# Kernel tuning notes

Hardware: AMD Instinct MI355X
Metric: run time of the kernel (lower is better)

The kernel has to match this reference:

```python
import jax, jax.numpy as jnp
import numpy as np

DEGREE = 10

def _chebyshev_basis(x, degree):
    # x: [B, F] -> basis: [B, F, degree+1] via T0=1, T1=t, Tk=2t*T_{k-1}-T_{k-2}
    t = jnp.tanh(x)
    polys = [jnp.ones_like(t), t]
    for _ in range(2, degree + 1):
        polys.append(2.0 * t * polys[-1] - polys[-2])
    return jnp.stack(polys, axis=-1)

def setup_inputs() -> dict:
    key = jax.random.key(0)
    k1, k2, k3, k4 = jax.random.split(key, 4)
    B, F_IN, F_OUT, D = 8192, 1024, 1024, DEGREE
    x = jax.random.normal(k1, (B, F_IN), dtype=jnp.float32)
    coeff_mean = jax.random.normal(k2, (F_IN, F_OUT, D + 1), dtype=jnp.float32) * 0.05
    coeff_log_var = jnp.full((F_IN, F_OUT, D + 1), -5.0, dtype=jnp.float32)
    base_weight = jax.random.normal(k3, (F_IN, F_OUT), dtype=jnp.float32) * 0.05
    # reparameterization noise, n_samples=1
    eps = jax.random.normal(k4, (1, F_IN, F_OUT, D + 1), dtype=jnp.float32)
    return {"x": x, "coeff_mean": coeff_mean, "coeff_log_var": coeff_log_var,
            "base_weight": base_weight, "eps": eps}

def reference(x, coeff_mean, coeff_log_var, base_weight, eps):
    basis = _chebyshev_basis(x, DEGREE)                      # [B, F_in, D+1]
    std = jnp.exp(0.5 * coeff_log_var)                       # [F_in, F_out, D+1]
    coeffs = coeff_mean[None] + eps * std[None]              # [S, F_in, F_out, D+1]
    poly_out = jnp.einsum('bin,sion->bo', basis, coeffs) / coeffs.shape[0]
    linear_out = x @ base_weight
    # KL with prior_mean=0, prior_var=1 (prior_scale=1.0)
    var = jnp.exp(coeff_log_var)
    kl = 0.5 * jnp.sum(var + coeff_mean ** 2 - 1.0 - coeff_log_var)
    return poly_out + linear_out, kl
```

## Files before the change

### kernel.cpp

```cpp
#include <hip/hip_runtime.h>

#define MDIM 8192
#define NDIM 1024
#define FIN  1024
#define DP1  11
#define KDIM 11264
#define KHALF 5632
#define ROWB 22528
#define HOFS 2883584u
#define FGOFS 1441792u
#define NT 88
#define NITER 44

typedef __attribute__((ext_vector_type(8))) short short8;
typedef __attribute__((ext_vector_type(4))) float float4v;
typedef const __attribute__((address_space(1))) unsigned int* gptr_t;
typedef __attribute__((address_space(3))) unsigned int* lptr_t;

__device__ __forceinline__ unsigned int pk2(float a, float b) {
  unsigned int ua = __float_as_uint(a), ub = __float_as_uint(b);
  ua += 0x7FFFu + ((ua >> 16) & 1u);
  ub += 0x7FFFu + ((ub >> 16) & 1u);
  return __builtin_amdgcn_perm(ub, ua, 0x07060302);
}

__device__ __forceinline__ float fast_tanh(float x) {
  float e = __expf(2.f * x);
  return 1.f - 2.f / (e + 1.f);
}

struct Cheb { float t, T2, T3, T4, T5, T6, T7, T8, T9, T10; };
__device__ __forceinline__ Cheb cheb_eval(float x) {
  Cheb c;
  c.t = fast_tanh(x);
  const float t2 = 2.f * c.t;
  c.T2 = t2 * c.t - 1.f;
  c.T3 = t2 * c.T2 - c.t;
  c.T4 = t2 * c.T3 - c.T2;
  c.T5 = t2 * c.T4 - c.T3;
  c.T6 = t2 * c.T5 - c.T4;
  c.T7 = t2 * c.T6 - c.T5;
  c.T8 = t2 * c.T7 - c.T6;
  c.T9 = t2 * c.T8 - c.T7;
  c.T10 = t2 * c.T9 - c.T8;
  return c;
}

__device__ __forceinline__ void pack_pair(float xa, float xb, unsigned int* w) {
  Cheb a = cheb_eval(xa), b = cheb_eval(xb);
  w[0] = pk2(a.t, a.T2);  w[1] = pk2(a.T3, a.T4); w[2] = pk2(a.T5, a.T6);
  w[3] = pk2(a.T7, a.T8); w[4] = pk2(a.T9, a.T10); w[5] = pk2(xa, b.t);
  w[6] = pk2(b.T2, b.T3); w[7] = pk2(b.T4, b.T5);  w[8] = pk2(b.T6, b.T7);
  w[9] = pk2(b.T8, b.T9); w[10] = pk2(b.T10, xb);
}

__global__ __launch_bounds__(256) void prep_A_kernel(const float* __restrict__ x,
                                                     unsigned int* __restrict__ A) {
  __shared__ unsigned int rowbuf[5632];
  const int row = blockIdx.x;
  const int tid = threadIdx.x;
  float4 xv = ((const float4*)(x + (size_t)row * FIN))[tid];
  unsigned int w[22];
  pack_pair(xv.x, xv.y, w);
  pack_pair(xv.z, xv.w, w + 11);
#pragma unroll
  for (int j = 0; j < 22; j++) rowbuf[tid * 22 + j] = w[j];
  __syncthreads();
  uint2* dst = (uint2*)((char*)A + (size_t)row * ROWB);
  const uint2* src = (const uint2*)rowbuf;
#pragma unroll
  for (int j = 0; j < 11; j++) dst[tid + j * 256] = src[tid + j * 256];
}

__global__ __launch_bounds__(256) void prep_B_kernel(const float4* __restrict__ mean4,
    const float4* __restrict__ lv4, const float* __restrict__ W,
    const float4* __restrict__ eps4, unsigned short* __restrict__ Bt,
    float* __restrict__ kl_out, float* __restrict__ bias) {
  __shared__ float cf[2816];
  __shared__ unsigned int pkb[5632];
  __shared__ float wsum[4];
  const int tid = threadIdx.x;
  const int g = blockIdx.x >> 3;
  const int po = blockIdx.x & 7;
  float klp = 0.f;
  float biasAcc = 0.f;
#pragma unroll 1
  for (int pr = 0; pr < 4; ++pr) {
#pragma unroll
    for (int f = 0; f < 2; ++f) {
      const int i = g * 8 + pr * 2 + f;
      const size_t b4 = (size_t)i * 2816 + po * 352;
#pragma unroll
      for (int qq = 0; qq < 2; ++qq) {
        const int idx = qq * 256 + tid;
        if (idx < 352) {
          float4 m = mean4[b4 + idx];
          float4 l = lv4[b4 + idx];
          float4 e = eps4[b4 + idx];
          float s0 = __expf(0.5f * l.x), s1 = __expf(0.5f * l.y);
          float s2 = __expf(0.5f * l.z), s3 = __expf(0.5f * l.w);
          float4 c;
          c.x = fmaf(e.x, s0, m.x); c.y = fmaf(e.y, s1, m.y);
          c.z = fmaf(e.z, s2, m.z); c.w = fmaf(e.w, s3, m.w);
          klp += (s0 * s0 + m.x * m.x - 1.f - l.x) + (s1 * s1 + m.y * m.y - 1.f - l.y)
               + (s2 * s2 + m.z * m.z - 1.f - l.z) + (s3 * s3 + m.w * m.w - 1.f - l.w);
          ((float4*)cf)[f * 352 + idx] = c;
        }
      }
    }
    __syncthreads();
    if (tid < 128) {
      const int o = tid;
      const float* ca = &cf[o * DP1];
      const float* cb = &cf[1408 + o * DP1];
      const float wa = W[(size_t)(g * 8 + pr * 2) * NDIM + po * 128 + o];
      const float wb = W[(size_t)(g * 8 + pr * 2 + 1) * NDIM + po * 128 + o];
      biasAcc += ca[0] + cb[0];
      unsigned int* dq = &pkb[o * 44 + pr * 11];
      dq[0] = pk2(ca[1], ca[2]); dq[1] = pk2(ca[3], ca[4]); dq[2] = pk2(ca[5], ca[6]);
      dq[3] = pk2(ca[7], ca[8]); dq[4] = pk2(ca[9], ca[10]); dq[5] = pk2(wa, cb[1]);
      dq[6] = pk2(cb[2], cb[3]); dq[7] = pk2(cb[4], cb[5]); dq[8] = pk2(cb[6], cb[7]);
      dq[9] = pk2(cb[8], cb[9]); dq[10] = pk2(cb[10], wb);
    }
    __syncthreads();
  }
#pragma unroll
  for (int it = 0; it < 6; ++it) {
    const int cc = it * 256 + tid;
    if (cc < 1408) {
      const int o = cc / 11, c = cc - o * 11;
      uint4 v = *(const uint4*)&pkb[o * 44 + c * 4];
      *(uint4*)((char*)Bt + (size_t)(po * 128 + o) * ROWB + g * 176 + c * 16) = v;
    }
  }
  if (tid < 128) atomicAdd(&bias[po * 128 + tid], biasAcc);
#pragma unroll
  for (int off = 32; off > 0; off >>= 1) klp += __shfl_down(klp, off, 64);
  if ((tid & 63) == 0) wsum[tid >> 6] = klp;
  __syncthreads();
  if (tid == 0) atomicAdd(kl_out, 0.5f * (wsum[0] + wsum[1] + wsum[2] + wsum[3]));
}

#define VMW(N) asm volatile("s_waitcnt vmcnt(" #N ")" ::: "memory")

#define STG_A(p, fg, t) do {                                                              \
    __builtin_amdgcn_global_load_lds((gptr_t)(gA + baseAlo + (fg) * FGOFS + (unsigned)(t) * 128u), \
        (lptr_t)(ldsp + (p) * 65536 + (fg) * 8192 + dA), 16, 0, 0);                       \
    __builtin_amdgcn_global_load_lds((gptr_t)(gA + baseAhi + (fg) * FGOFS + (unsigned)(t) * 128u), \
        (lptr_t)(ldsp + (p) * 65536 + 16384 + (fg) * 8192 + dA), 16, 0, 0);               \
  } while (0)

#define STG_B(p, h, t) do {                                                               \
    __builtin_amdgcn_global_load_lds((gptr_t)(gB + baseB0 + (h) * HOFS + (unsigned)(t) * 128u), \
        (lptr_t)(ldsp + (p) * 65536 + 32768 + (h) * 16384 + dA), 16, 0, 0);               \
    __builtin_amdgcn_global_load_lds((gptr_t)(gB + baseB1 + (h) * HOFS + (unsigned)(t) * 128u), \
        (lptr_t)(ldsp + (p) * 65536 + 32768 + (h) * 16384 + 8192 + dA), 16, 0, 0);        \
  } while (0)

#define PH(p, f, STG_STMT, WAIT_STMT) do {                                                \
    const char* ap_ = ldsp + (p) * 65536 + aBase + (f) * 4096;                            \
    short8 a00 = *(const short8*)(ap_ + offk0);                                           \
    short8 a01 = *(const short8*)(ap_ + offk1);                                           \
    short8 a10 = *(const short8*)(ap_ + 2048 + offk0);                                    \
    short8 a11 = *(const short8*)(ap_ + 2048 + offk1);                                    \
    if ((f) == 0) {                                                                       \
      const char* bp_ = ldsp + (p) * 65536 + bBase;                                       \
      bfr[0][0] = *(const short8*)(bp_ + offk0);        bfr[0][1] = *(const short8*)(bp_ + offk1); \
      bfr[1][0] = *(const short8*)(bp_ + 2048 + offk0); bfr[1][1] = *(const short8*)(bp_ + 2048 + offk1); \
      bfr[2][0] = *(const short8*)(bp_ + 4096 + offk0); bfr[2][1] = *(const short8*)(bp_ + 4096 + offk1); \
      bfr[3][0] = *(const short8*)(bp_ + 6144 + offk0); bfr[3][1] = *(const short8*)(bp_ + 6144 + offk1); \
    }                                                                                     \
    STG_STMT;                                                                             \
    WAIT_STMT;                                                                            \
    __builtin_amdgcn_sched_barrier(0);                                                    \
    __builtin_amdgcn_s_barrier();                                                         \
    __builtin_amdgcn_sched_barrier(0);                                                    \
    __builtin_amdgcn_s_setprio(1);                                                        \
    _Pragma("unroll")                                                                     \
    for (int n_ = 0; n_ < 4; ++n_) {                                                      \
      acc[2 * (f)][n_]     = __builtin_amdgcn_mfma_f32_16x16x32_bf16(a00, bfr[n_][0], acc[2 * (f)][n_], 0, 0, 0);     \
      acc[2 * (f)][n_]     = __builtin_amdgcn_mfma_f32_16x16x32_bf16(a01, bfr[n_][1], acc[2 * (f)][n_], 0, 0, 0);     \
      acc[2 * (f) + 1][n_] = __builtin_amdgcn_mfma_f32_16x16x32_bf16(a10, bfr[n_][0], acc[2 * (f) + 1][n_], 0, 0, 0); \
      acc[2 * (f) + 1][n_] = __builtin_amdgcn_mfma_f32_16x16x32_bf16(a11, bfr[n_][1], acc[2 * (f) + 1][n_], 0, 0, 0); \
    }                                                                                     \
    __builtin_amdgcn_s_setprio(0);                                                        \
  } while (0)

__global__ __launch_bounds__(512, 2) void gemm_kernel(const unsigned short* __restrict__ A,
    const unsigned short* __restrict__ Bt, const float* __restrict__ bias,
    float* __restrict__ C) {
  __shared__ char lds[131072];
  char* ldsp = (char*)lds;
  const int tid = threadIdx.x;
  const int lane = tid & 63;
  const int wid = tid >> 6;
  const int wr = wid >> 2;
  const int wc = wid & 3;
  const int q = lane >> 4;
  const int r = lane & 15;
  const int bid = blockIdx.x;
  const int nt_ = bid & 3;
  const int kh = (bid >> 2) & 1;
  const int mt = bid >> 3;
  const int gm0 = mt * 256;
  const int gn0 = nt_ * 256;
  const unsigned kbyte0 = (unsigned)kh * KHALF * 2;

  const char* gA = (const char*)A;
  const char* gB = (const char*)Bt;

  const int srow = tid >> 3;
  const int scol = ((tid & 7) ^ (srow & 7)) << 4;
  const unsigned baseAlo = (unsigned)(gm0 + srow) * ROWB + kbyte0 + scol;
  const unsigned baseAhi = baseAlo + 128u * ROWB;
  const unsigned baseB0  = (unsigned)(gn0 + srow) * ROWB + kbyte0 + scol;
  const unsigned baseB1  = (unsigned)(gn0 + 64 + srow) * ROWB + kbyte0 + scol;
  const int dA = tid * 16;

  const int s7 = r & 7;
  const int offk0 = ((q ^ s7) << 4);
  const int offk1 = (((q + 4) ^ s7) << 4);
  const int aBase = wr * 16384 + r * 128;
  const int bBase = 32768 + (wc >> 1) * 16384 + ((wc & 1) * 64 + r) * 128;

  float4v acc[8][4];
#pragma unroll
  for (int m = 0; m < 8; m++)
#pragma unroll
    for (int n = 0; n < 4; n++) acc[m][n] = (float4v){0.f, 0.f, 0.f, 0.f};
  short8 bfr[4][2];

  STG_A(0, 0, 0); STG_A(0, 1, 0); STG_B(0, 0, 0); STG_B(0, 1, 0);
  STG_B(1, 0, 1); STG_B(1, 1, 1);
  VMW(4);
  __builtin_amdgcn_sched_barrier(0);
  __builtin_amdgcn_s_barrier();
  __builtin_amdgcn_sched_barrier(0);

#pragma unroll 1
  for (int i = 0; i < NITER - 1; ++i) {
    const int t1 = 2 * i + 1, t2 = 2 * i + 2, t3 = 2 * i + 3;
    PH(0, 0, STG_A(1, 0, t1), ;);
    PH(0, 1, STG_A(1, 1, t1), ;);
    PH(0, 2, STG_B(0, 0, t2), ;);
    PH(0, 3, STG_B(0, 1, t2), VMW(4));
    PH(1, 0, STG_A(0, 0, t2), ;);
    PH(1, 1, STG_A(0, 1, t2), ;);
    PH(1, 2, STG_B(1, 0, t3), ;);
    PH(1, 3, STG_B(1, 1, t3), VMW(4));
  }
  PH(0, 0, STG_A(1, 0, NT - 1), ;);
  PH(0, 1, STG_A(1, 1, NT - 1), ;);
  PH(0, 2, ;, ;);
  PH(0, 3, ;, VMW(0));
  PH(1, 0, ;, ;);
  PH(1, 1, ;, ;);
  PH(1, 2, ;, ;);
  PH(1, 3, ;, ;);

  float bv[4] = {0.f, 0.f, 0.f, 0.f};
  if (kh == 0) {
    const float* bp = bias + gn0 + wc * 64 + r;
#pragma unroll
    for (int n = 0; n < 4; n++) bv[n] = bp[n * 16];
  }
  float* Cb = C + (size_t)(gm0 + wr * 128) * NDIM + (gn0 + wc * 64);
#pragma unroll
  for (int m = 0; m < 8; m++)
#pragma unroll
    for (int n = 0; n < 4; n++)
#pragma unroll
      for (int v = 0; v < 4; v++)
        atomicAdd(&Cb[(size_t)(m * 16 + q * 4 + v) * NDIM + (n * 16 + r)], acc[m][n][v] + bv[n]);
}

extern "C" void kernel_launch(void* const* d_in, const int* in_sizes, int n_in,
                              void* d_out, int out_size, void* d_ws, size_t ws_size,
                              hipStream_t stream) {
  const float* x    = (const float*)d_in[0];
  const float* mean = (const float*)d_in[1];
  const float* lv   = (const float*)d_in[2];
  const float* W    = (const float*)d_in[3];
  const float* eps  = (const float*)d_in[4];
  float* out = (float*)d_out;

  unsigned short* Abf = (unsigned short*)d_ws;
  unsigned short* Bt  = (unsigned short*)((char*)d_ws + (size_t)MDIM * ROWB);
  float* bias = (float*)((char*)d_ws + (size_t)MDIM * ROWB + (size_t)NDIM * ROWB);
  float* kl = out + (size_t)MDIM * NDIM;

  hipMemsetAsync(out, 0, ((size_t)MDIM * NDIM + 1) * sizeof(float), stream);
  hipMemsetAsync(bias, 0, NDIM * sizeof(float), stream);
  prep_A_kernel<<<MDIM, 256, 0, stream>>>(x, (unsigned int*)Abf);
  prep_B_kernel<<<1024, 256, 0, stream>>>((const float4*)mean, (const float4*)lv, W,
                                          (const float4*)eps, Bt, kl, bias);
  gemm_kernel<<<256, 512, 0, stream>>>(Abf, Bt, bias, out);
}
```

Before: 413.0 us.

## Merge prep kernels, replace atomic epilogue with split-K stores plus final add

Fuses the A and B preparation kernels into one launch that branches on block index. The GEMM no longer issues float atomics into a zeroed output. The second K-half stores fp32 directly, the first K-half stores a bf16 partial to workspace, and a new elementwise kernel adds the partial and the bias into the output. This drops the large output memset and the atomic traffic, and the LDS fragment loads and MFMA order are also interleaved differently. In exchange it adds an extra launch and a full read-modify-write pass, and rounding the first half's partial to bf16 loses precision.

```diff
diff --git a/kernel.cpp b/kernel.cpp
--- a/kernel.cpp
+++ b/kernel.cpp
@@ -22,6 +22,12 @@
   ua += 0x7FFFu + ((ua >> 16) & 1u);
   ub += 0x7FFFu + ((ub >> 16) & 1u);
   return __builtin_amdgcn_perm(ub, ua, 0x07060302);
+}
+
+__device__ __forceinline__ unsigned short bf16rne(float a) {
+  unsigned int u = __float_as_uint(a);
+  u += 0x7FFFu + ((u >> 16) & 1u);
+  return (unsigned short)(u >> 16);
 }
 
 __device__ __forceinline__ float fast_tanh(float x) {
@@ -54,32 +60,32 @@
   w[9] = pk2(b.T8, b.T9); w[10] = pk2(b.T10, xb);
 }
 
-__global__ __launch_bounds__(256) void prep_A_kernel(const float* __restrict__ x,
-                                                     unsigned int* __restrict__ A) {
-  __shared__ unsigned int rowbuf[5632];
-  const int row = blockIdx.x;
-  const int tid = threadIdx.x;
-  float4 xv = ((const float4*)(x + (size_t)row * FIN))[tid];
-  unsigned int w[22];
-  pack_pair(xv.x, xv.y, w);
-  pack_pair(xv.z, xv.w, w + 11);
-#pragma unroll
-  for (int j = 0; j < 22; j++) rowbuf[tid * 22 + j] = w[j];
-  __syncthreads();
-  uint2* dst = (uint2*)((char*)A + (size_t)row * ROWB);
-  const uint2* src = (const uint2*)rowbuf;
-#pragma unroll
-  for (int j = 0; j < 11; j++) dst[tid + j * 256] = src[tid + j * 256];
-}
-
-__global__ __launch_bounds__(256) void prep_B_kernel(const float4* __restrict__ mean4,
+__global__ __launch_bounds__(256) void prep_kernel(const float* __restrict__ x,
+    unsigned int* __restrict__ A, const float4* __restrict__ mean4,
     const float4* __restrict__ lv4, const float* __restrict__ W,
     const float4* __restrict__ eps4, unsigned short* __restrict__ Bt,
     float* __restrict__ kl_out, float* __restrict__ bias) {
-  __shared__ float cf[2816];
-  __shared__ unsigned int pkb[5632];
-  __shared__ float wsum[4];
+  __shared__ __align__(16) char smem[33824];
   const int tid = threadIdx.x;
+  if (blockIdx.x >= 1024) {
+    unsigned int* rowbuf = (unsigned int*)smem;
+    const int row = blockIdx.x - 1024;
+    float4 xv = ((const float4*)(x + (size_t)row * FIN))[tid];
+    unsigned int w[22];
+    pack_pair(xv.x, xv.y, w);
+    pack_pair(xv.z, xv.w, w + 11);
+#pragma unroll
+    for (int j = 0; j < 22; j++) rowbuf[tid * 22 + j] = w[j];
+    __syncthreads();
+    uint2* dst = (uint2*)((char*)A + (size_t)row * ROWB);
+    const uint2* src = (const uint2*)rowbuf;
+#pragma unroll
+    for (int j = 0; j < 11; j++) dst[tid + j * 256] = src[tid + j * 256];
+    return;
+  }
+  float* cf = (float*)smem;
+  unsigned int* pkb = (unsigned int*)(smem + 11264);
+  float* wsum = (float*)(smem + 33792);
   const int g = blockIdx.x >> 3;
   const int po = blockIdx.x & 7;
   float klp = 0.f;
@@ -159,17 +165,24 @@
 
 #define PH(p, f, STG_STMT, WAIT_STMT) do {                                                \
     const char* ap_ = ldsp + (p) * 65536 + aBase + (f) * 4096;                            \
-    short8 a00 = *(const short8*)(ap_ + offk0);                                           \
-    short8 a01 = *(const short8*)(ap_ + offk1);                                           \
-    short8 a10 = *(const short8*)(ap_ + 2048 + offk0);                                    \
-    short8 a11 = *(const short8*)(ap_ + 2048 + offk1);                                    \
     if ((f) == 0) {                                                                       \
       const char* bp_ = ldsp + (p) * 65536 + bBase;                                       \
-      bfr[0][0] = *(const short8*)(bp_ + offk0);        bfr[0][1] = *(const short8*)(bp_ + offk1); \
-      bfr[1][0] = *(const short8*)(bp_ + 2048 + offk0); bfr[1][1] = *(const short8*)(bp_ + 2048 + offk1); \
-      bfr[2][0] = *(const short8*)(bp_ + 4096 + offk0); bfr[2][1] = *(const short8*)(bp_ + 4096 + offk1); \
-      bfr[3][0] = *(const short8*)(bp_ + 6144 + offk0); bfr[3][1] = *(const short8*)(bp_ + 6144 + offk1); \
+      bfr[0][0] = *(const short8*)(bp_ + offk0);                                          \
+      bfr[1][0] = *(const short8*)(bp_ + 2048 + offk0);                                   \
+      bfr[2][0] = *(const short8*)(bp_ + 4096 + offk0);                                   \
+      bfr[3][0] = *(const short8*)(bp_ + 6144 + offk0);                                   \
     }                                                                                     \
+    short8 a00 = *(const short8*)(ap_ + offk0);                                           \
+    short8 a10 = *(const short8*)(ap_ + 2048 + offk0);                                    \
+    if ((f) == 0) {                                                                       \
+      const char* bp_ = ldsp + (p) * 65536 + bBase;                                       \
+      bfr[0][1] = *(const short8*)(bp_ + offk1);                                          \
+      bfr[1][1] = *(const short8*)(bp_ + 2048 + offk1);                                   \
+      bfr[2][1] = *(const short8*)(bp_ + 4096 + offk1);                                   \
+      bfr[3][1] = *(const short8*)(bp_ + 6144 + offk1);                                   \
+    }                                                                                     \
+    short8 a01 = *(const short8*)(ap_ + offk1);                                           \
+    short8 a11 = *(const short8*)(ap_ + 2048 + offk1);                                    \
     STG_STMT;                                                                             \
     WAIT_STMT;                                                                            \
     __builtin_amdgcn_sched_barrier(0);                                                    \
@@ -179,16 +192,19 @@
     _Pragma("unroll")                                                                     \
     for (int n_ = 0; n_ < 4; ++n_) {                                                      \
       acc[2 * (f)][n_]     = __builtin_amdgcn_mfma_f32_16x16x32_bf16(a00, bfr[n_][0], acc[2 * (f)][n_], 0, 0, 0);     \
+      acc[2 * (f) + 1][n_] = __builtin_amdgcn_mfma_f32_16x16x32_bf16(a10, bfr[n_][0], acc[2 * (f) + 1][n_], 0, 0, 0); \
+    }                                                                                     \
+    _Pragma("unroll")                                                                     \
+    for (int n_ = 0; n_ < 4; ++n_) {                                                      \
       acc[2 * (f)][n_]     = __builtin_amdgcn_mfma_f32_16x16x32_bf16(a01, bfr[n_][1], acc[2 * (f)][n_], 0, 0, 0);     \
-      acc[2 * (f) + 1][n_] = __builtin_amdgcn_mfma_f32_16x16x32_bf16(a10, bfr[n_][0], acc[2 * (f) + 1][n_], 0, 0, 0); \
       acc[2 * (f) + 1][n_] = __builtin_amdgcn_mfma_f32_16x16x32_bf16(a11, bfr[n_][1], acc[2 * (f) + 1][n_], 0, 0, 0); \
     }                                                                                     \
     __builtin_amdgcn_s_setprio(0);                                                        \
   } while (0)
 
 __global__ __launch_bounds__(512, 2) void gemm_kernel(const unsigned short* __restrict__ A,
-    const unsigned short* __restrict__ Bt, const float* __restrict__ bias,
-    float* __restrict__ C) {
+    const unsigned short* __restrict__ Bt, float* __restrict__ C,
+    unsigned short* __restrict__ C0) {
   __shared__ char lds[131072];
   char* ldsp = (char*)lds;
   const int tid = threadIdx.x;
@@ -258,20 +274,47 @@
   PH(1, 2, ;, ;);
   PH(1, 3, ;, ;);
 
-  float bv[4] = {0.f, 0.f, 0.f, 0.f};
-  if (kh == 0) {
-    const float* bp = bias + gn0 + wc * 64 + r;
-#pragma unroll
-    for (int n = 0; n < 4; n++) bv[n] = bp[n * 16];
-  }
-  float* Cb = C + (size_t)(gm0 + wr * 128) * NDIM + (gn0 + wc * 64);
-#pragma unroll
-  for (int m = 0; m < 8; m++)
-#pragma unroll
-    for (int n = 0; n < 4; n++)
-#pragma unroll
-      for (int v = 0; v < 4; v++)
-        atomicAdd(&Cb[(size_t)(m * 16 + q * 4 + v) * NDIM + (n * 16 + r)], acc[m][n][v] + bv[n]);
+  if (kh) {
+    float* Cb = C + (size_t)(gm0 + wr * 128) * NDIM + (gn0 + wc * 64);
+#pragma unroll
+    for (int m = 0; m < 8; m++)
+#pragma unroll
+      for (int n = 0; n < 4; n++)
+#pragma unroll
+        for (int v = 0; v < 4; v++)
+          Cb[(size_t)(m * 16 + q * 4 + v) * NDIM + (n * 16 + r)] = acc[m][n][v];
+  } else {
+    unsigned short* Pb = C0 + (size_t)(gm0 + wr * 128) * NDIM + (gn0 + wc * 64);
+#pragma unroll
+    for (int m = 0; m < 8; m++)
+#pragma unroll
+      for (int n = 0; n < 4; n++)
+#pragma unroll
+        for (int v = 0; v < 4; v++)
+          Pb[(size_t)(m * 16 + q * 4 + v) * NDIM + (n * 16 + r)] = bf16rne(acc[m][n][v]);
+  }
+}
+
+__global__ __launch_bounds__(256) void final_add_kernel(float* __restrict__ out,
+    const unsigned short* __restrict__ C0, const float* __restrict__ bias) {
+  const size_t base = ((size_t)blockIdx.x * 256 + threadIdx.x) * 8;
+  const int col = (int)(base & 1023);
+  float4 b0 = *(const float4*)(bias + col);
+  float4 b1 = *(const float4*)(bias + col + 4);
+  float4 o0 = *(const float4*)(out + base);
+  float4 o1 = *(const float4*)(out + base + 4);
+  ushort4 p0 = *(const ushort4*)(C0 + base);
+  ushort4 p1 = *(const ushort4*)(C0 + base + 4);
+  o0.x += __uint_as_float((unsigned)p0.x << 16) + b0.x;
+  o0.y += __uint_as_float((unsigned)p0.y << 16) + b0.y;
+  o0.z += __uint_as_float((unsigned)p0.z << 16) + b0.z;
+  o0.w += __uint_as_float((unsigned)p0.w << 16) + b0.w;
+  o1.x += __uint_as_float((unsigned)p1.x << 16) + b1.x;
+  o1.y += __uint_as_float((unsigned)p1.y << 16) + b1.y;
+  o1.z += __uint_as_float((unsigned)p1.z << 16) + b1.z;
+  o1.w += __uint_as_float((unsigned)p1.w << 16) + b1.w;
+  *(float4*)(out + base) = o0;
+  *(float4*)(out + base + 4) = o1;
 }
 
 extern "C" void kernel_launch(void* const* d_in, const int* in_sizes, int n_in,
@@ -287,12 +330,14 @@
   unsigned short* Abf = (unsigned short*)d_ws;
   unsigned short* Bt  = (unsigned short*)((char*)d_ws + (size_t)MDIM * ROWB);
   float* bias = (float*)((char*)d_ws + (size_t)MDIM * ROWB + (size_t)NDIM * ROWB);
+  unsigned short* C0 = (unsigned short*)((char*)bias + 4096);
   float* kl = out + (size_t)MDIM * NDIM;
 
-  hipMemsetAsync(out, 0, ((size_t)MDIM * NDIM + 1) * sizeof(float), stream);
   hipMemsetAsync(bias, 0, NDIM * sizeof(float), stream);
-  prep_A_kernel<<<MDIM, 256, 0, stream>>>(x, (unsigned int*)Abf);
-  prep_B_kernel<<<1024, 256, 0, stream>>>((const float4*)mean, (const float4*)lv, W,
-                                          (const float4*)eps, Bt, kl, bias);
-  gemm_kernel<<<256, 512, 0, stream>>>(Abf, Bt, bias, out);
-}
+  hipMemsetAsync(kl, 0, sizeof(float), stream);
+  prep_kernel<<<9216, 256, 0, stream>>>(x, (unsigned int*)Abf, (const float4*)mean,
+                                        (const float4*)lv, W, (const float4*)eps,
+                                        Bt, kl, bias);
+  gemm_kernel<<<256, 512, 0, stream>>>(Abf, Bt, out, C0);
+  final_add_kernel<<<4096, 256, 0, stream>>>(out, C0, bias);
+}
```

Result: faster. 381.2 us (-7.7%).
